# Performance work log

Hardware: AMD Instinct MI355X
Metric: run time of the kernel (lower is better)

## Reference

```python
import jax, jax.numpy as jnp
import numpy as np

N_NODES = 50000
N_EDGES = 800000
IN_FEAT = 128
HID = 128
OUT = 10
N_GRAPHS = 128
BN_EPS = 1e-5


def setup_inputs() -> dict:
    key = jax.random.key(0)
    ks = jax.random.split(key, 16)
    inp = {
        "n_feat": jax.random.normal(ks[0], (N_NODES, IN_FEAT), dtype=jnp.float32),
        "src": jax.random.randint(ks[1], (N_EDGES,), 0, N_NODES),
        "dst": jax.random.randint(ks[2], (N_EDGES,), 0, N_NODES),
        "graph_ids": jnp.sort(jax.random.randint(ks[3], (N_NODES,), 0, N_GRAPHS)),
        # GraphConv weights (DGL layout: weight [in, out], bias [out])
        "W1": jax.random.normal(ks[4], (IN_FEAT, HID), dtype=jnp.float32) / np.sqrt(IN_FEAT),
        "b1": jnp.zeros((HID,), dtype=jnp.float32),
        "W2": jax.random.normal(ks[5], (HID, HID), dtype=jnp.float32) / np.sqrt(HID),
        "b2": jnp.zeros((HID,), dtype=jnp.float32),
        # BatchNorm1d affine params
        "gamma": jnp.ones((HID,), dtype=jnp.float32),
        "beta": jnp.zeros((HID,), dtype=jnp.float32),
        # MLP head
        "fc1_w": jax.random.normal(ks[6], (HID, HID), dtype=jnp.float32) / np.sqrt(HID),
        "fc1_b": jnp.zeros((HID,), dtype=jnp.float32),
        "fc2_w": jax.random.normal(ks[7], (HID, OUT), dtype=jnp.float32) / np.sqrt(HID),
        "fc2_b": jnp.zeros((OUT,), dtype=jnp.float32),
    }
    return inp


def _graph_conv(x, W, b, src, dst, inv_sqrt_out, inv_sqrt_in):
    # DGL GraphConv, norm='both': h = D_in^{-1/2} A D_out^{-1/2} x W + b
    h = x * inv_sqrt_out[:, None]          # [N, d_in]
    h = h @ W                              # [N, d_out] (project before gather: fewer bytes moved)
    agg = jax.ops.segment_sum(h[src], dst, num_segments=N_NODES)  # gather + scatter-add
    return agg * inv_sqrt_in[:, None] + b


def reference(n_feat, src, dst, graph_ids, W1, b1, W2, b2, gamma, beta,
              fc1_w, fc1_b, fc2_w, fc2_b):
    ones_e = jnp.ones((N_EDGES,), dtype=jnp.float32)
    deg_out = jnp.clip(jax.ops.segment_sum(ones_e, src, num_segments=N_NODES), 1.0)
    deg_in = jnp.clip(jax.ops.segment_sum(ones_e, dst, num_segments=N_NODES), 1.0)
    inv_sqrt_out = jax.lax.rsqrt(deg_out)
    inv_sqrt_in = jax.lax.rsqrt(deg_in)

    x = jax.nn.relu(_graph_conv(n_feat, W1, b1, src, dst, inv_sqrt_out, inv_sqrt_in))
    # dropout is identity in eval mode
    x = jax.nn.relu(_graph_conv(x, W2, b2, src, dst, inv_sqrt_out, inv_sqrt_in))

    # SumPooling over graphs
    embedding = jax.ops.segment_sum(x, graph_ids, num_segments=N_GRAPHS)  # [B, HID]

    # BatchNorm1d (training-mode batch stats, biased variance like torch)
    mu = jnp.mean(embedding, axis=0)
    var = jnp.mean(jnp.square(embedding - mu), axis=0)
    h = gamma * (embedding - mu) * jax.lax.rsqrt(var + BN_EPS) + beta

    h = jax.nn.relu(h @ fc1_w + fc1_b)
    logits = h @ fc2_w + fc2_b
    return embedding, jax.nn.log_softmax(logits, axis=-1)
```

## Files before the change

### kernel.cpp

```cpp
#include <hip/hip_runtime.h>
#include <hip/hip_bf16.h>
#include <math.h>

#define N_NODES 50000
#define N_EDGES 800000
#define HID 128
#define N_GRAPHS 128
#define OUTC 10
#define BN_EPS 1e-5f

#define SCAN_B 256
#define N_SCAN_BLOCKS ((N_NODES + SCAN_B - 1) / SCAN_B)

#define POOL_CHUNK 32
#define N_POOL_BLOCKS ((N_NODES + POOL_CHUNK - 1) / POOL_CHUNK)

#define HB 80
#define HWORDS (N_NODES / 2)
#define HR_B 128
#define HR_BLOCKS ((HWORDS + HR_B - 1) / HR_B)

#define EPAD 8
#define E_SRC_CAP (N_EDGES + N_NODES * EPAD)

#define LDA 136

#define MM_BLOCKS ((N_NODES + 64) / 64)

typedef short short8 __attribute__((ext_vector_type(8)));
typedef float floatx4 __attribute__((ext_vector_type(4)));

template <typename T, typename F>
__device__ inline T bitcast(F f) {
    union { F a; T b; } u;
    u.a = f;
    return u.b;
}

__device__ inline unsigned short f2bf(float x) {
    return __hip_bfloat16_raw(__float2bfloat16(x)).x;
}

__global__ __launch_bounds__(1024) void hist_part_kernel(const int* __restrict__ src,
                                                         const int* __restrict__ dst,
                                                         unsigned int* __restrict__ part,
                                                         const float* __restrict__ W1,
                                                         const float* __restrict__ W2,
                                                         unsigned short* __restrict__ Wp) {
    if (blockIdx.x == 2 * HB) {
        for (int q = threadIdx.x; q < 4096; q += 1024) {
            int wi = q >> 11;
            const float* __restrict__ W = wi ? W2 : W1;
            int t2 = q & 2047;
            int tile = t2 >> 6, lane = t2 & 63;
            int kc = tile >> 3, nt = tile & 7;
            int n = lane & 15, quad = lane >> 4;
            unsigned short v[8];
#pragma unroll
            for (int j = 0; j < 8; j++) {
                int k = kc * 32 + quad * 8 + j;
                v[j] = f2bf(W[k * HID + nt * 16 + n]);
            }
            *(uint4*)&Wp[(size_t)q * 8] = *(uint4*)v;
        }
        return;
    }
    __shared__ unsigned int h[HWORDS];
    for (int i = threadIdx.x; i < HWORDS; i += 1024) h[i] = 0;
    __syncthreads();
    int half = (blockIdx.x >= HB) ? 1 : 0;
    const int* __restrict__ idx = half ? dst : src;
    int b = blockIdx.x - half * HB;
    for (int e = b * 1024 + threadIdx.x; e < N_EDGES; e += HB * 1024) {
        int v = idx[e];
        atomicAdd(&h[v >> 1], 1u << ((v & 1) << 4));
    }
    __syncthreads();
    unsigned int* __restrict__ out = part + (size_t)blockIdx.x * HWORDS;
    for (int i = threadIdx.x; i < HWORDS; i += 1024) out[i] = h[i];
}

__global__ __launch_bounds__(HR_B) void hist_reduce_kernel(unsigned int* __restrict__ part,
                                                           int* __restrict__ cnt_in,
                                                           float* __restrict__ inv_out,
                                                           float* __restrict__ inv_in,
                                                           int* __restrict__ bsum) {
    int w = blockIdx.x * HR_B + threadIdx.x;
    int padsum = 0;
    if (w < HWORDS) {
        unsigned int s = 0, d = 0;
        for (int b = 0; b < HB; b++) {
            s += part[(size_t)b * HWORDS + w];
            unsigned int c = part[(size_t)(b + HB) * HWORDS + w];
            part[(size_t)(b + HB) * HWORDS + w] = d;
            d += c;
        }
        int i0 = w * 2, i1 = i0 + 1;
        int so0 = (int)(s & 0xFFFFu), so1 = (int)(s >> 16);
        int di0 = (int)(d & 0xFFFFu), di1 = (int)(d >> 16);
        cnt_in[i0] = di0;
        cnt_in[i1] = di1;
        inv_out[i0] = rsqrtf(fmaxf((float)so0, 1.0f));
        inv_out[i1] = rsqrtf(fmaxf((float)so1, 1.0f));
        inv_in[i0] = rsqrtf(fmaxf((float)di0, 1.0f));
        inv_in[i1] = rsqrtf(fmaxf((float)di1, 1.0f));
        padsum = ((di0 + EPAD - 1) & ~(EPAD - 1)) + ((di1 + EPAD - 1) & ~(EPAD - 1));
    }
    __shared__ int red[HR_B];
    red[threadIdx.x] = padsum;
    __syncthreads();
    for (int o = HR_B / 2; o > 0; o >>= 1) {
        if (threadIdx.x < o) red[threadIdx.x] += red[threadIdx.x + o];
        __syncthreads();
    }
    if (threadIdx.x == 0) bsum[blockIdx.x] = red[0];
}

__device__ inline void mm_tail(const unsigned short* __restrict__ xs,
                               const unsigned short* __restrict__ Wp,
                               __hip_bfloat16* __restrict__ Y, int row0) {
    int tid = threadIdx.x;
    int wave = tid >> 6, lane = tid & 63;
    int m = lane & 15, quad = lane >> 4;
    int rowl = wave * 16;

    short8 a[4];
#pragma unroll
    for (int kc = 0; kc < 4; kc++)
        a[kc] = bitcast<short8>(*(const uint4*)&xs[(rowl + m) * LDA + kc * 32 + quad * 8]);

    floatx4 acc[8];
#pragma unroll
    for (int nt = 0; nt < 8; nt++) acc[nt] = (floatx4){0.f, 0.f, 0.f, 0.f};

#pragma unroll
    for (int nt = 0; nt < 8; nt++) {
#pragma unroll
        for (int kc = 0; kc < 4; kc++) {
            short8 bfr = bitcast<short8>(
                *(const uint4*)&Wp[((size_t)(kc * 8 + nt) * 64 + lane) * 8]);
            acc[nt] = __builtin_amdgcn_mfma_f32_16x16x32_bf16(a[kc], bfr, acc[nt], 0, 0, 0);
        }
    }

#pragma unroll
    for (int nt = 0; nt < 8; nt++) {
#pragma unroll
        for (int i = 0; i < 4; i++) {
            int rg = row0 + rowl + quad * 4 + i;
            if (rg < N_NODES + 1) {
                Y[(size_t)rg * HID + nt * 16 + m] = __float2bfloat16(acc[nt][i]);
            }
        }
    }
}

__global__ __launch_bounds__(256) void scanmm1_kernel(const int* __restrict__ cnt,
                                                      const int* __restrict__ bsum,
                                                      int* __restrict__ row_ptr,
                                                      int* __restrict__ edge_src,
                                                      const float* __restrict__ X,
                                                      const float* __restrict__ scale,
                                                      const unsigned short* __restrict__ Wp,
                                                      __hip_bfloat16* __restrict__ Y,
                                                      float* __restrict__ emb) {
    __shared__ unsigned short xs[64 * LDA];
    int t = threadIdx.x;
    int b = blockIdx.x;

    if (b >= N_SCAN_BLOCKS) {
        if (b == N_SCAN_BLOCKS + MM_BLOCKS) {
            for (int i = t; i < N_GRAPHS * HID; i += 256) emb[i] = 0.f;
            return;
        }
        int row0 = (b - N_SCAN_BLOCKS) * 64;
        for (int j = 0; j < 8; j++) {
            int idx4 = j * 256 + t;
            int r = idx4 >> 5;
            int col = (idx4 & 31) * 4;
            int rg = row0 + r;
            float4 v = make_float4(0.f, 0.f, 0.f, 0.f);
            if (rg < N_NODES) {
                v = *(const float4*)&X[(size_t)rg * HID + col];
                float sc = scale[rg];
                v.x *= sc; v.y *= sc; v.z *= sc; v.w *= sc;
            }
            unsigned short o[4];
            o[0] = f2bf(v.x); o[1] = f2bf(v.y); o[2] = f2bf(v.z); o[3] = f2bf(v.w);
            *(ushort4*)&xs[r * LDA + col] = *(ushort4*)o;
        }
        __syncthreads();
        mm_tail(xs, Wp, Y, row0);
        return;
    }

    int* sb = (int*)xs;
    int* part = (int*)xs + 256;
    sb[t] = (t < N_SCAN_BLOCKS) ? bsum[t] : 0;
    __syncthreads();
    for (int off = 1; off < SCAN_B; off <<= 1) {
        int u = (t >= off) ? sb[t - off] : 0;
        __syncthreads();
        sb[t] += u;
        __syncthreads();
    }
    int boff = (b == 0) ? 0 : sb[b - 1];

    int i = b * SCAN_B + t;
    int raw = (i < N_NODES) ? cnt[i] : 0;
    int v = (raw + EPAD - 1) & ~(EPAD - 1);
    part[t] = v;
    __syncthreads();
    for (int off = 1; off < SCAN_B; off <<= 1) {
        int u = (t >= off) ? part[t - off] : 0;
        __syncthreads();
        part[t] += u;
        __syncthreads();
    }
    if (i < N_NODES) {
        int ex = part[t] - v + boff;
        row_ptr[i] = ex;
        for (int p = ex + raw; p < ex + v; p++) edge_src[p] = N_NODES;
        if (i == N_NODES - 1) row_ptr[N_NODES] = ex + v;
    }
}

__global__ __launch_bounds__(1024) void csr_fill_kernel(const int* __restrict__ src,
                                                        const int* __restrict__ dst,
                                                        const unsigned int* __restrict__ part,
                                                        const int* __restrict__ row_ptr,
                                                        int* __restrict__ edge_src) {
    __shared__ unsigned int loc[HWORDS];
    int b = blockIdx.x;
    const unsigned int* __restrict__ off = part + (size_t)(b + HB) * HWORDS;
    for (int i = threadIdx.x; i < HWORDS; i += 1024) loc[i] = off[i];
    __syncthreads();
    for (int e = b * 1024 + threadIdx.x; e < N_EDGES; e += HB * 1024) {
        int d = dst[e];
        unsigned int old = atomicAdd(&loc[d >> 1], 1u << ((d & 1) << 4));
        int local = (d & 1) ? (int)(old >> 16) : (int)(old & 0xFFFFu);
        edge_src[row_ptr[d] + local] = src[e];
    }
}

__global__ __launch_bounds__(256) void matmul_bf16_kernel(const __hip_bfloat16* __restrict__ Xb,
                                                          const unsigned short* __restrict__ Wp,
                                                          __hip_bfloat16* __restrict__ Y) {
    __shared__ unsigned short xs[64 * LDA];
    int tid = threadIdx.x;
    int row0 = blockIdx.x * 64;
    for (int j = 0; j < 4; j++) {
        int idx8 = j * 256 + tid;
        int r = idx8 >> 4;
        int c = (idx8 & 15) * 8;
        int rg = row0 + r;
        uint4 v = make_uint4(0u, 0u, 0u, 0u);
        if (rg < N_NODES) v = *(const uint4*)&Xb[(size_t)rg * HID + c];
        *(uint4*)&xs[r * LDA + c] = v;
    }
    __syncthreads();
    mm_tail(xs, Wp, Y, row0);
}

#define ACC8(u)                                                                              \
    acc[0] += __uint_as_float(u.x << 16); acc[1] += __uint_as_float(u.x & 0xFFFF0000u);      \
    acc[2] += __uint_as_float(u.y << 16); acc[3] += __uint_as_float(u.y & 0xFFFF0000u);      \
    acc[4] += __uint_as_float(u.z << 16); acc[5] += __uint_as_float(u.z & 0xFFFF0000u);      \
    acc[6] += __uint_as_float(u.w << 16); acc[7] += __uint_as_float(u.w & 0xFFFF0000u);

template <bool BF16OUT>
__global__ __launch_bounds__(256) void agg_kernel_t(const __hip_bfloat16* __restrict__ Y,
                                                    const int* __restrict__ edge_src,
                                                    const int* __restrict__ row_ptr,
                                                    const float* __restrict__ inv_in,
                                                    const float* __restrict__ inv_out,
                                                    const float* __restrict__ bias,
                                                    void* __restrict__ Xout) {
    const uint4* __restrict__ Yq = (const uint4*)Y;
    int wave = threadIdx.x >> 6;
    int lane = threadIdx.x & 63;
    int n = blockIdx.x * 4 + wave;
    if (n >= N_NODES) return;
    int beg = row_ptr[n], end = row_ptr[n + 1];
    int esub = lane >> 4;
    int f16  = lane & 15;
    float acc[8] = {};
    for (int base = beg; base < end; base += 64) {
        int mm = min(64, end - base);
        int idx = (lane < mm) ? edge_src[base + lane] : N_NODES;
        int j = 0;
        for (; j + 16 <= mm; j += 16) {
            int s0 = __shfl(idx, j + esub);
            int s1 = __shfl(idx, j + 4 + esub);
            int s2 = __shfl(idx, j + 8 + esub);
            int s3 = __shfl(idx, j + 12 + esub);
            uint4 u0 = Yq[s0 * (HID / 8) + f16];
            uint4 u1 = Yq[s1 * (HID / 8) + f16];
            uint4 u2 = Yq[s2 * (HID / 8) + f16];
            uint4 u3 = Yq[s3 * (HID / 8) + f16];
            ACC8(u0); ACC8(u1); ACC8(u2); ACC8(u3);
        }
        if (j < mm) {
            int s0 = __shfl(idx, j + esub);
            int s1 = __shfl(idx, j + 4 + esub);
            uint4 u0 = Yq[s0 * (HID / 8) + f16];
            uint4 u1 = Yq[s1 * (HID / 8) + f16];
            ACC8(u0); ACC8(u1);
        }
    }
#pragma unroll
    for (int i = 0; i < 8; i++) {
        acc[i] += __shfl_xor(acc[i], 16);
        acc[i] += __shfl_xor(acc[i], 32);
    }
    if (lane < 16) {
        float si = inv_in[n];
        int f0 = f16 * 8;
        float4 b0 = *(const float4*)&bias[f0];
        float4 b1 = *(const float4*)&bias[f0 + 4];
        float o[8];
        o[0] = fmaxf(acc[0] * si + b0.x, 0.f);
        o[1] = fmaxf(acc[1] * si + b0.y, 0.f);
        o[2] = fmaxf(acc[2] * si + b0.z, 0.f);
        o[3] = fmaxf(acc[3] * si + b0.w, 0.f);
        o[4] = fmaxf(acc[4] * si + b1.x, 0.f);
        o[5] = fmaxf(acc[5] * si + b1.y, 0.f);
        o[6] = fmaxf(acc[6] * si + b1.z, 0.f);
        o[7] = fmaxf(acc[7] * si + b1.w, 0.f);
        if constexpr (BF16OUT) {
            float so = inv_out[n];
            unsigned short u[8];
#pragma unroll
            for (int i = 0; i < 8; i++) u[i] = f2bf(o[i] * so);
            *(uint4*)&((__hip_bfloat16*)Xout)[(size_t)n * HID + f0] = *(uint4*)u;
        } else {
            float* Xf = (float*)Xout;
            *(float4*)&Xf[(size_t)n * HID + f0] = make_float4(o[0], o[1], o[2], o[3]);
            *(float4*)&Xf[(size_t)n * HID + f0 + 4] = make_float4(o[4], o[5], o[6], o[7]);
        }
    }
}

__global__ __launch_bounds__(64) void pool_kernel(const float* __restrict__ X,
                                                  const int* __restrict__ gid,
                                                  float* __restrict__ emb) {
    int lane = threadIdx.x;
    int n0 = blockIdx.x * POOL_CHUNK;
    int n1 = min(n0 + POOL_CHUNK, N_NODES);
    if (n0 >= N_NODES) return;
    int g_cur = gid[n0];
    float ax = 0.f, ay = 0.f;
    for (int n = n0; n < n1; n++) {
        int g = gid[n];
        if (g != g_cur) {
            atomicAdd(&emb[g_cur * HID + lane * 2], ax);
            atomicAdd(&emb[g_cur * HID + lane * 2 + 1], ay);
            ax = 0.f; ay = 0.f;
            g_cur = g;
        }
        float2 v = *(const float2*)&X[(size_t)n * HID + lane * 2];
        ax += v.x;
        ay += v.y;
    }
    atomicAdd(&emb[g_cur * HID + lane * 2], ax);
    atomicAdd(&emb[g_cur * HID + lane * 2 + 1], ay);
}

__global__ __launch_bounds__(128) void head_fused_kernel(const float* __restrict__ emb,
                                                         const float* __restrict__ gamma,
                                                         const float* __restrict__ beta,
                                                         const float* __restrict__ fc1_w,
                                                         const float* __restrict__ fc1_b,
                                                         const float* __restrict__ fc2_w,
                                                         const float* __restrict__ fc2_b,
                                                         float* __restrict__ out) {
    int r = blockIdx.x, f = threadIdx.x;
    float s = 0.f;
    for (int row = 0; row < N_GRAPHS; row++) s += emb[row * HID + f];
    float mu = s * (1.f / N_GRAPHS);
    float v = 0.f;
    for (int row = 0; row < N_GRAPHS; row++) {
        float d = emb[row * HID + f] - mu;
        v += d * d;
    }
    v *= (1.f / N_GRAPHS);
    float sc = gamma[f] * rsqrtf(v + BN_EPS);
    float sh = beta[f] - mu * sc;

    __shared__ float xr[HID];
    xr[f] = emb[r * HID + f] * sc + sh;
    __syncthreads();
    float acc = fc1_b[f];
    for (int k = 0; k < HID; k++) acc += xr[k] * fc1_w[k * HID + f];
    __shared__ float hr[HID];
    hr[f] = fmaxf(acc, 0.f);
    __syncthreads();

    __shared__ float logits[OUTC];
    __shared__ float mstat[2];
    if (f < OUTC) {
        float a = fc2_b[f];
        for (int k = 0; k < HID; k++) a += hr[k] * fc2_w[k * OUTC + f];
        logits[f] = a;
    }
    __syncthreads();
    if (f == 0) {
        float m = logits[0];
        for (int o = 1; o < OUTC; o++) m = fmaxf(m, logits[o]);
        float sum = 0.f;
        for (int o = 0; o < OUTC; o++) sum += expf(logits[o] - m);
        mstat[0] = m;
        mstat[1] = logf(sum);
    }
    __syncthreads();
    if (f < OUTC) out[r * OUTC + f] = logits[f] - mstat[0] - mstat[1];
}

extern "C" void kernel_launch(void* const* d_in, const int* in_sizes, int n_in,
                              void* d_out, int out_size, void* d_ws, size_t ws_size,
                              hipStream_t stream) {
    const float* n_feat = (const float*)d_in[0];
    const int*   src    = (const int*)d_in[1];
    const int*   dst    = (const int*)d_in[2];
    const int*   gid    = (const int*)d_in[3];
    const float* W1     = (const float*)d_in[4];
    const float* b1     = (const float*)d_in[5];
    const float* W2     = (const float*)d_in[6];
    const float* b2     = (const float*)d_in[7];
    const float* gamma  = (const float*)d_in[8];
    const float* beta   = (const float*)d_in[9];
    const float* fc1_w  = (const float*)d_in[10];
    const float* fc1_b  = (const float*)d_in[11];
    const float* fc2_w  = (const float*)d_in[12];
    const float* fc2_b  = (const float*)d_in[13];

    char* wsb = (char*)d_ws;
    size_t off = 0;
    auto alloc = [&](size_t bytes) -> void* {
        void* p = wsb + off;
        off += (bytes + 255) & ~(size_t)255;
        return p;
    };
    int*   cnt_in  = (int*)alloc((size_t)N_NODES * 4);
    int*   row_ptr = (int*)alloc((size_t)(N_NODES + 1) * 4);
    int*   e_src   = (int*)alloc((size_t)E_SRC_CAP * 4);
    float* inv_out = (float*)alloc((size_t)N_NODES * 4);
    float* inv_in  = (float*)alloc((size_t)N_NODES * 4);
    unsigned int* part = (unsigned int*)alloc((size_t)2 * HB * HWORDS * 4);
    __hip_bfloat16* Y  = (__hip_bfloat16*)alloc((size_t)(N_NODES + 1) * HID * 2);
    float* X       = (float*)alloc((size_t)N_NODES * HID * 4);
    __hip_bfloat16* X1b = (__hip_bfloat16*)alloc((size_t)N_NODES * HID * 2);
    unsigned short* Wp = (unsigned short*)alloc((size_t)2 * 32 * 64 * 8 * 2);
    int*   bsum    = (int*)alloc((size_t)SCAN_B * 4);

    float* emb_out = (float*)d_out;
    float* lsm_out = emb_out + N_GRAPHS * HID;

    hist_part_kernel<<<2 * HB + 1, 1024, 0, stream>>>(src, dst, part, W1, W2, Wp);
    hist_reduce_kernel<<<HR_BLOCKS, HR_B, 0, stream>>>(part, cnt_in, inv_out, inv_in, bsum);
    scanmm1_kernel<<<N_SCAN_BLOCKS + MM_BLOCKS + 1, 256, 0, stream>>>(
        cnt_in, bsum, row_ptr, e_src, n_feat, inv_out, Wp, Y, emb_out);
    csr_fill_kernel<<<HB, 1024, 0, stream>>>(src, dst, part, row_ptr, e_src);

    agg_kernel_t<true><<<(N_NODES + 3) / 4, 256, 0, stream>>>(Y, e_src, row_ptr, inv_in,
                                                              inv_out, b1, X1b);
    matmul_bf16_kernel<<<MM_BLOCKS, 256, 0, stream>>>(X1b, Wp + (size_t)32 * 64 * 8, Y);
    agg_kernel_t<false><<<(N_NODES + 3) / 4, 256, 0, stream>>>(Y, e_src, row_ptr, inv_in,
                                                               nullptr, b2, X);

    pool_kernel<<<N_POOL_BLOCKS, 64, 0, stream>>>(X, gid, emb_out);
    head_fused_kernel<<<N_GRAPHS, HID, 0, stream>>>(emb_out, gamma, beta, fc1_w, fc1_b,
                                                    fc2_w, fc2_b, lsm_out);
}
```

Before: 244.7 us.

## Fuse layer-1 aggregation with layer-2 matmul and co-schedule CSR fill with matmul1

Fuses the first aggregation with the second GEMM. Each 16-node block aggregates into shared memory and then runs MFMA against W2, so the bf16 intermediate X1b no longer makes a global round trip and one launch is dropped. The scan moves to its own kernel, and the CSR fill is merged with the first matmul into one 1024-thread launch so the two independent stages can overlap. The costs are more shared-memory pressure from the 1024-thread, 320-row tiles and reduced parallelism in the fused aggregation block.

```diff
diff --git a/kernel.cpp b/kernel.cpp
--- a/kernel.cpp
+++ b/kernel.cpp
@@ -25,7 +25,12 @@
 
 #define LDA 136
 
-#define MM_BLOCKS ((N_NODES + 64) / 64)
+#define MM1_ROWS 320
+#define MM1_SLICES (MM1_ROWS / 16)
+#define MM1_TILES ((N_NODES + 1 + MM1_ROWS - 1) / MM1_ROWS)
+
+#define AGG_NODES 16
+#define AGG_BLOCKS (N_NODES / AGG_NODES)
 
 typedef short short8 __attribute__((ext_vector_type(8)));
 typedef float floatx4 __attribute__((ext_vector_type(4)));
@@ -116,13 +121,45 @@
     if (threadIdx.x == 0) bsum[blockIdx.x] = red[0];
 }
 
-__device__ inline void mm_tail(const unsigned short* __restrict__ xs,
-                               const unsigned short* __restrict__ Wp,
-                               __hip_bfloat16* __restrict__ Y, int row0) {
-    int tid = threadIdx.x;
-    int wave = tid >> 6, lane = tid & 63;
+__global__ void scan_write_kernel(const int* __restrict__ cnt, const int* __restrict__ bsum,
+                                  int* __restrict__ row_ptr, int* __restrict__ edge_src) {
+    __shared__ int sb[SCAN_B];
+    __shared__ int part[SCAN_B];
+    int t = threadIdx.x;
+    sb[t] = (t < N_SCAN_BLOCKS) ? bsum[t] : 0;
+    __syncthreads();
+    for (int off = 1; off < SCAN_B; off <<= 1) {
+        int u = (t >= off) ? sb[t - off] : 0;
+        __syncthreads();
+        sb[t] += u;
+        __syncthreads();
+    }
+    int boff = (blockIdx.x == 0) ? 0 : sb[blockIdx.x - 1];
+
+    int i = blockIdx.x * SCAN_B + t;
+    int raw = (i < N_NODES) ? cnt[i] : 0;
+    int v = (raw + EPAD - 1) & ~(EPAD - 1);
+    part[t] = v;
+    __syncthreads();
+    for (int off = 1; off < SCAN_B; off <<= 1) {
+        int u = (t >= off) ? part[t - off] : 0;
+        __syncthreads();
+        part[t] += u;
+        __syncthreads();
+    }
+    if (i < N_NODES) {
+        int ex = part[t] - v + boff;
+        row_ptr[i] = ex;
+        for (int p = ex + raw; p < ex + v; p++) edge_src[p] = N_NODES;
+        if (i == N_NODES - 1) row_ptr[N_NODES] = ex + v;
+    }
+}
+
+__device__ inline void mm_slice16(const unsigned short* __restrict__ xs,
+                                  const unsigned short* __restrict__ Wp,
+                                  __hip_bfloat16* __restrict__ Y, int row0, int rowl) {
+    int lane = threadIdx.x & 63;
     int m = lane & 15, quad = lane >> 4;
-    int rowl = wave * 16;
 
     short8 a[4];
 #pragma unroll
@@ -155,111 +192,58 @@
     }
 }
 
-__global__ __launch_bounds__(256) void scanmm1_kernel(const int* __restrict__ cnt,
-                                                      const int* __restrict__ bsum,
-                                                      int* __restrict__ row_ptr,
+__global__ __launch_bounds__(1024) void csrmm1_kernel(const int* __restrict__ src,
+                                                      const int* __restrict__ dst,
+                                                      const unsigned int* __restrict__ part,
+                                                      const int* __restrict__ row_ptr,
                                                       int* __restrict__ edge_src,
                                                       const float* __restrict__ X,
                                                       const float* __restrict__ scale,
                                                       const unsigned short* __restrict__ Wp,
                                                       __hip_bfloat16* __restrict__ Y,
                                                       float* __restrict__ emb) {
-    __shared__ unsigned short xs[64 * LDA];
-    int t = threadIdx.x;
-    int b = blockIdx.x;
-
-    if (b >= N_SCAN_BLOCKS) {
-        if (b == N_SCAN_BLOCKS + MM_BLOCKS) {
-            for (int i = t; i < N_GRAPHS * HID; i += 256) emb[i] = 0.f;
-            return;
-        }
-        int row0 = (b - N_SCAN_BLOCKS) * 64;
-        for (int j = 0; j < 8; j++) {
-            int idx4 = j * 256 + t;
-            int r = idx4 >> 5;
-            int col = (idx4 & 31) * 4;
-            int rg = row0 + r;
-            float4 v = make_float4(0.f, 0.f, 0.f, 0.f);
-            if (rg < N_NODES) {
-                v = *(const float4*)&X[(size_t)rg * HID + col];
-                float sc = scale[rg];
-                v.x *= sc; v.y *= sc; v.z *= sc; v.w *= sc;
-            }
-            unsigned short o[4];
-            o[0] = f2bf(v.x); o[1] = f2bf(v.y); o[2] = f2bf(v.z); o[3] = f2bf(v.w);
-            *(ushort4*)&xs[r * LDA + col] = *(ushort4*)o;
-        }
+    __shared__ unsigned int shb[HWORDS];
+    int t = threadIdx.x, b = blockIdx.x;
+
+    if (b < HB) {
+        unsigned int* loc = shb;
+        const unsigned int* __restrict__ off = part + (size_t)(b + HB) * HWORDS;
+        for (int i = t; i < HWORDS; i += 1024) loc[i] = off[i];
         __syncthreads();
-        mm_tail(xs, Wp, Y, row0);
+        for (int e = b * 1024 + t; e < N_EDGES; e += HB * 1024) {
+            int d = dst[e];
+            unsigned int old = atomicAdd(&loc[d >> 1], 1u << ((d & 1) << 4));
+            int local = (d & 1) ? (int)(old >> 16) : (int)(old & 0xFFFFu);
+            edge_src[row_ptr[d] + local] = src[e];
+        }
         return;
     }
-
-    int* sb = (int*)xs;
-    int* part = (int*)xs + 256;
-    sb[t] = (t < N_SCAN_BLOCKS) ? bsum[t] : 0;
-    __syncthreads();
-    for (int off = 1; off < SCAN_B; off <<= 1) {
-        int u = (t >= off) ? sb[t - off] : 0;
-        __syncthreads();
-        sb[t] += u;
-        __syncthreads();
-    }
-    int boff = (b == 0) ? 0 : sb[b - 1];
-
-    int i = b * SCAN_B + t;
-    int raw = (i < N_NODES) ? cnt[i] : 0;
-    int v = (raw + EPAD - 1) & ~(EPAD - 1);
-    part[t] = v;
-    __syncthreads();
-    for (int off = 1; off < SCAN_B; off <<= 1) {
-        int u = (t >= off) ? part[t - off] : 0;
-        __syncthreads();
-        part[t] += u;
-        __syncthreads();
-    }
-    if (i < N_NODES) {
-        int ex = part[t] - v + boff;
-        row_ptr[i] = ex;
-        for (int p = ex + raw; p < ex + v; p++) edge_src[p] = N_NODES;
-        if (i == N_NODES - 1) row_ptr[N_NODES] = ex + v;
-    }
-}
-
-__global__ __launch_bounds__(1024) void csr_fill_kernel(const int* __restrict__ src,
-                                                        const int* __restrict__ dst,
-                                                        const unsigned int* __restrict__ part,
-                                                        const int* __restrict__ row_ptr,
-                                                        int* __restrict__ edge_src) {
-    __shared__ unsigned int loc[HWORDS];
-    int b = blockIdx.x;
-    const unsigned int* __restrict__ off = part + (size_t)(b + HB) * HWORDS;
-    for (int i = threadIdx.x; i < HWORDS; i += 1024) loc[i] = off[i];
-    __syncthreads();
-    for (int e = b * 1024 + threadIdx.x; e < N_EDGES; e += HB * 1024) {
-        int d = dst[e];
-        unsigned int old = atomicAdd(&loc[d >> 1], 1u << ((d & 1) << 4));
-        int local = (d & 1) ? (int)(old >> 16) : (int)(old & 0xFFFFu);
-        edge_src[row_ptr[d] + local] = src[e];
-    }
-}
-
-__global__ __launch_bounds__(256) void matmul_bf16_kernel(const __hip_bfloat16* __restrict__ Xb,
-                                                          const unsigned short* __restrict__ Wp,
-                                                          __hip_bfloat16* __restrict__ Y) {
-    __shared__ unsigned short xs[64 * LDA];
-    int tid = threadIdx.x;
-    int row0 = blockIdx.x * 64;
-    for (int j = 0; j < 4; j++) {
-        int idx8 = j * 256 + tid;
-        int r = idx8 >> 4;
-        int c = (idx8 & 15) * 8;
+    if (b == HB + MM1_TILES) {
+        for (int i = t; i < N_GRAPHS * HID; i += 1024) emb[i] = 0.f;
+        return;
+    }
+
+    unsigned short* xs = (unsigned short*)shb;
+    int row0 = (b - HB) * MM1_ROWS;
+    for (int j = 0; j < MM1_ROWS / 32; j++) {
+        int idx4 = j * 1024 + t;
+        int r = idx4 >> 5;
+        int col = (idx4 & 31) * 4;
         int rg = row0 + r;
-        uint4 v = make_uint4(0u, 0u, 0u, 0u);
-        if (rg < N_NODES) v = *(const uint4*)&Xb[(size_t)rg * HID + c];
-        *(uint4*)&xs[r * LDA + c] = v;
-    }
-    __syncthreads();
-    mm_tail(xs, Wp, Y, row0);
+        float4 v = make_float4(0.f, 0.f, 0.f, 0.f);
+        if (rg < N_NODES) {
+            v = *(const float4*)&X[(size_t)rg * HID + col];
+            float sc = scale[rg];
+            v.x *= sc; v.y *= sc; v.z *= sc; v.w *= sc;
+        }
+        unsigned short o[4];
+        o[0] = f2bf(v.x); o[1] = f2bf(v.y); o[2] = f2bf(v.z); o[3] = f2bf(v.w);
+        *(ushort4*)&xs[r * LDA + col] = *(ushort4*)o;
+    }
+    __syncthreads();
+    int wave = t >> 6;
+    for (int sl = wave; sl < MM1_SLICES; sl += 16)
+        mm_slice16(xs, Wp, Y, row0, sl * 16);
 }
 
 #define ACC8(u)                                                                              \
@@ -268,14 +252,109 @@
     acc[4] += __uint_as_float(u.z << 16); acc[5] += __uint_as_float(u.z & 0xFFFF0000u);      \
     acc[6] += __uint_as_float(u.w << 16); acc[7] += __uint_as_float(u.w & 0xFFFF0000u);
 
-template <bool BF16OUT>
-__global__ __launch_bounds__(256) void agg_kernel_t(const __hip_bfloat16* __restrict__ Y,
-                                                    const int* __restrict__ edge_src,
-                                                    const int* __restrict__ row_ptr,
-                                                    const float* __restrict__ inv_in,
-                                                    const float* __restrict__ inv_out,
-                                                    const float* __restrict__ bias,
-                                                    void* __restrict__ Xout) {
+__global__ __launch_bounds__(256) void agg1mm2_kernel(const __hip_bfloat16* __restrict__ Y1,
+                                                      const int* __restrict__ edge_src,
+                                                      const int* __restrict__ row_ptr,
+                                                      const float* __restrict__ inv_in,
+                                                      const float* __restrict__ inv_out,
+                                                      const float* __restrict__ bias,
+                                                      const unsigned short* __restrict__ Wp2,
+                                                      __hip_bfloat16* __restrict__ Y2) {
+    if (blockIdx.x == AGG_BLOCKS) {
+        if (threadIdx.x < 16) {
+            uint4 z = make_uint4(0u, 0u, 0u, 0u);
+            *(uint4*)&Y2[(size_t)N_NODES * HID + threadIdx.x * 8] = z;
+        }
+        return;
+    }
+    __shared__ unsigned short xs[AGG_NODES * LDA];
+    const uint4* __restrict__ Yq = (const uint4*)Y1;
+    int wave = threadIdx.x >> 6;
+    int lane = threadIdx.x & 63;
+    int esub = lane >> 4;
+    int f16 = lane & 15;
+
+    for (int it = 0; it < 4; it++) {
+        int n = blockIdx.x * AGG_NODES + wave * 4 + it;
+        int beg = row_ptr[n], end = row_ptr[n + 1];
+        float acc[8] = {};
+        for (int base = beg; base < end; base += 64) {
+            int mm = min(64, end - base);
+            int idx = (lane < mm) ? edge_src[base + lane] : N_NODES;
+            int j = 0;
+            for (; j + 16 <= mm; j += 16) {
+                int s0 = __shfl(idx, j + esub);
+                int s1 = __shfl(idx, j + 4 + esub);
+                int s2 = __shfl(idx, j + 8 + esub);
+                int s3 = __shfl(idx, j + 12 + esub);
+                uint4 u0 = Yq[s0 * (HID / 8) + f16];
+                uint4 u1 = Yq[s1 * (HID / 8) + f16];
+                uint4 u2 = Yq[s2 * (HID / 8) + f16];
+                uint4 u3 = Yq[s3 * (HID / 8) + f16];
+                ACC8(u0); ACC8(u1); ACC8(u2); ACC8(u3);
+            }
+            if (j < mm) {
+                int s0 = __shfl(idx, j + esub);
+                int s1 = __shfl(idx, j + 4 + esub);
+                uint4 u0 = Yq[s0 * (HID / 8) + f16];
+                uint4 u1 = Yq[s1 * (HID / 8) + f16];
+                ACC8(u0); ACC8(u1);
+            }
+        }
+#pragma unroll
+        for (int i = 0; i < 8; i++) {
+            acc[i] += __shfl_xor(acc[i], 16);
+            acc[i] += __shfl_xor(acc[i], 32);
+        }
+        if (lane < 16) {
+            float si = inv_in[n];
+            float so = inv_out[n];
+            int f0 = f16 * 8;
+            float4 b0 = *(const float4*)&bias[f0];
+            float4 b1 = *(const float4*)&bias[f0 + 4];
+            unsigned short u[8];
+            u[0] = f2bf(fmaxf(acc[0] * si + b0.x, 0.f) * so);
+            u[1] = f2bf(fmaxf(acc[1] * si + b0.y, 0.f) * so);
+            u[2] = f2bf(fmaxf(acc[2] * si + b0.z, 0.f) * so);
+            u[3] = f2bf(fmaxf(acc[3] * si + b0.w, 0.f) * so);
+            u[4] = f2bf(fmaxf(acc[4] * si + b1.x, 0.f) * so);
+            u[5] = f2bf(fmaxf(acc[5] * si + b1.y, 0.f) * so);
+            u[6] = f2bf(fmaxf(acc[6] * si + b1.z, 0.f) * so);
+            u[7] = f2bf(fmaxf(acc[7] * si + b1.w, 0.f) * so);
+            *(uint4*)&xs[(wave * 4 + it) * LDA + f0] = *(uint4*)u;
+        }
+    }
+    __syncthreads();
+
+    int m = lane & 15, quad = lane >> 4;
+    short8 a[4];
+#pragma unroll
+    for (int kc = 0; kc < 4; kc++)
+        a[kc] = bitcast<short8>(*(const uint4*)&xs[m * LDA + kc * 32 + quad * 8]);
+#pragma unroll
+    for (int w2 = 0; w2 < 2; w2++) {
+        int nt = wave * 2 + w2;
+        floatx4 acc2 = (floatx4){0.f, 0.f, 0.f, 0.f};
+#pragma unroll
+        for (int kc = 0; kc < 4; kc++) {
+            short8 bfr = bitcast<short8>(
+                *(const uint4*)&Wp2[((size_t)(kc * 8 + nt) * 64 + lane) * 8]);
+            acc2 = __builtin_amdgcn_mfma_f32_16x16x32_bf16(a[kc], bfr, acc2, 0, 0, 0);
+        }
+#pragma unroll
+        for (int i = 0; i < 4; i++) {
+            int rg = blockIdx.x * AGG_NODES + quad * 4 + i;
+            Y2[(size_t)rg * HID + nt * 16 + m] = __float2bfloat16(acc2[i]);
+        }
+    }
+}
+
+__global__ __launch_bounds__(256) void agg2_kernel(const __hip_bfloat16* __restrict__ Y,
+                                                   const int* __restrict__ edge_src,
+                                                   const int* __restrict__ row_ptr,
+                                                   const float* __restrict__ inv_in,
+                                                   const float* __restrict__ bias,
+                                                   float* __restrict__ Xout) {
     const uint4* __restrict__ Yq = (const uint4*)Y;
     int wave = threadIdx.x >> 6;
     int lane = threadIdx.x & 63;
@@ -283,7 +362,7 @@
     if (n >= N_NODES) return;
     int beg = row_ptr[n], end = row_ptr[n + 1];
     int esub = lane >> 4;
-    int f16  = lane & 15;
+    int f16 = lane & 15;
     float acc[8] = {};
     for (int base = beg; base < end; base += 64) {
         int mm = min(64, end - base);
@@ -318,26 +397,17 @@
         int f0 = f16 * 8;
         float4 b0 = *(const float4*)&bias[f0];
         float4 b1 = *(const float4*)&bias[f0 + 4];
-        float o[8];
-        o[0] = fmaxf(acc[0] * si + b0.x, 0.f);
-        o[1] = fmaxf(acc[1] * si + b0.y, 0.f);
-        o[2] = fmaxf(acc[2] * si + b0.z, 0.f);
-        o[3] = fmaxf(acc[3] * si + b0.w, 0.f);
-        o[4] = fmaxf(acc[4] * si + b1.x, 0.f);
-        o[5] = fmaxf(acc[5] * si + b1.y, 0.f);
-        o[6] = fmaxf(acc[6] * si + b1.z, 0.f);
-        o[7] = fmaxf(acc[7] * si + b1.w, 0.f);
-        if constexpr (BF16OUT) {
-            float so = inv_out[n];
-            unsigned short u[8];
-#pragma unroll
-            for (int i = 0; i < 8; i++) u[i] = f2bf(o[i] * so);
-            *(uint4*)&((__hip_bfloat16*)Xout)[(size_t)n * HID + f0] = *(uint4*)u;
-        } else {
-            float* Xf = (float*)Xout;
-            *(float4*)&Xf[(size_t)n * HID + f0] = make_float4(o[0], o[1], o[2], o[3]);
-            *(float4*)&Xf[(size_t)n * HID + f0 + 4] = make_float4(o[4], o[5], o[6], o[7]);
-        }
+        float4 o0, o1;
+        o0.x = fmaxf(acc[0] * si + b0.x, 0.f);
+        o0.y = fmaxf(acc[1] * si + b0.y, 0.f);
+        o0.z = fmaxf(acc[2] * si + b0.z, 0.f);
+        o0.w = fmaxf(acc[3] * si + b0.w, 0.f);
+        o1.x = fmaxf(acc[4] * si + b1.x, 0.f);
+        o1.y = fmaxf(acc[5] * si + b1.y, 0.f);
+        o1.z = fmaxf(acc[6] * si + b1.z, 0.f);
+        o1.w = fmaxf(acc[7] * si + b1.w, 0.f);
+        *(float4*)&Xout[(size_t)n * HID + f0] = o0;
+        *(float4*)&Xout[(size_t)n * HID + f0 + 4] = o1;
     }
 }
 
@@ -447,9 +517,9 @@
     float* inv_out = (float*)alloc((size_t)N_NODES * 4);
     float* inv_in  = (float*)alloc((size_t)N_NODES * 4);
     unsigned int* part = (unsigned int*)alloc((size_t)2 * HB * HWORDS * 4);
-    __hip_bfloat16* Y  = (__hip_bfloat16*)alloc((size_t)(N_NODES + 1) * HID * 2);
+    __hip_bfloat16* Y1 = (__hip_bfloat16*)alloc((size_t)(N_NODES + 1) * HID * 2);
+    __hip_bfloat16* Y2 = (__hip_bfloat16*)alloc((size_t)(N_NODES + 1) * HID * 2);
     float* X       = (float*)alloc((size_t)N_NODES * HID * 4);
-    __hip_bfloat16* X1b = (__hip_bfloat16*)alloc((size_t)N_NODES * HID * 2);
     unsigned short* Wp = (unsigned short*)alloc((size_t)2 * 32 * 64 * 8 * 2);
     int*   bsum    = (int*)alloc((size_t)SCAN_B * 4);
 
@@ -458,15 +528,12 @@
 
     hist_part_kernel<<<2 * HB + 1, 1024, 0, stream>>>(src, dst, part, W1, W2, Wp);
     hist_reduce_kernel<<<HR_BLOCKS, HR_B, 0, stream>>>(part, cnt_in, inv_out, inv_in, bsum);
-    scanmm1_kernel<<<N_SCAN_BLOCKS + MM_BLOCKS + 1, 256, 0, stream>>>(
-        cnt_in, bsum, row_ptr, e_src, n_feat, inv_out, Wp, Y, emb_out);
-    csr_fill_kernel<<<HB, 1024, 0, stream>>>(src, dst, part, row_ptr, e_src);
-
-    agg_kernel_t<true><<<(N_NODES + 3) / 4, 256, 0, stream>>>(Y, e_src, row_ptr, inv_in,
-                                                              inv_out, b1, X1b);
-    matmul_bf16_kernel<<<MM_BLOCKS, 256, 0, stream>>>(X1b, Wp + (size_t)32 * 64 * 8, Y);
-    agg_kernel_t<false><<<(N_NODES + 3) / 4, 256, 0, stream>>>(Y, e_src, row_ptr, inv_in,
-                                                               nullptr, b2, X);
+    scan_write_kernel<<<N_SCAN_BLOCKS, SCAN_B, 0, stream>>>(cnt_in, bsum, row_ptr, e_src);
+    csrmm1_kernel<<<HB + MM1_TILES + 1, 1024, 0, stream>>>(src, dst, part, row_ptr, e_src,
+                                                           n_feat, inv_out, Wp, Y1, emb_out);
+    agg1mm2_kernel<<<AGG_BLOCKS + 1, 256, 0, stream>>>(Y1, e_src, row_ptr, inv_in, inv_out,
+                                                       b1, Wp + (size_t)32 * 64 * 8, Y2);
+    agg2_kernel<<<(N_NODES + 3) / 4, 256, 0, stream>>>(Y2, e_src, row_ptr, inv_in, b2, X);
 
     pool_kernel<<<N_POOL_BLOCKS, 64, 0, stream>>>(X, gid, emb_out);
     head_fused_kernel<<<N_GRAPHS, HID, 0, stream>>>(emb_out, gamma, beta, fc1_w, fc1_b,
```

Result: slower. 257.7 us (+5.3%).
